# Kernel optimization log

Hardware: AMD Instinct MI355X
Metric: run time of the kernel (lower is better)

Reference implementation:

```python
import jax, jax.numpy as jnp
import numpy as np

N_FUNC, N_API = 200000, 50000
E = 400000
H = 64
L = 2


def _mean_agg(x_src, edge_index, num_dst):
    # gather source features along edges, scatter-mean onto destination nodes
    src, dst = edge_index[0], edge_index[1]
    s = jax.ops.segment_sum(x_src[src], dst, num_segments=num_dst)
    cnt = jax.ops.segment_sum(jnp.ones((dst.shape[0], 1), x_src.dtype), dst, num_segments=num_dst)
    return s / jnp.maximum(cnt, 1.0)  # zero for isolated nodes (PyG scatter-mean behavior)


def setup_inputs() -> dict:
    key = jax.random.key(0)
    ks = jax.random.split(key, 32)
    s = 0.1  # weight init scale
    inp = {
        "x_func": jax.random.normal(ks[0], (N_FUNC, 128), jnp.float32),
        "x_api": jax.random.normal(ks[1], (N_API, 64), jnp.float32),
        # input projections per node type
        "w_in_func": jax.random.normal(ks[2], (H, 128), jnp.float32) * s,
        "b_in_func": jnp.zeros((H,), jnp.float32),
        "w_in_api": jax.random.normal(ks[3], (H, 64), jnp.float32) * s,
        "b_in_api": jnp.zeros((H,), jnp.float32),
        # SAGEConv params, stacked over num_layers: lin_l (W,b) applied to aggregated msgs, lin_r (no bias) on dst
        "Wl_calls": jax.random.normal(ks[4], (L, H, H), jnp.float32) * s,
        "bl_calls": jnp.zeros((L, H), jnp.float32),
        "Wr_calls": jax.random.normal(ks[5], (L, H, H), jnp.float32) * s,
        "Wl_uses": jax.random.normal(ks[6], (L, H, H), jnp.float32) * s,
        "bl_uses": jnp.zeros((L, H), jnp.float32),
        "Wr_uses": jax.random.normal(ks[7], (L, H, H), jnp.float32) * s,
        "Wl_usedby": jax.random.normal(ks[8], (L, H, H), jnp.float32) * s,
        "bl_usedby": jnp.zeros((L, H), jnp.float32),
        "Wr_usedby": jax.random.normal(ks[9], (L, H, H), jnp.float32) * s,
        # classifier: Linear(2H -> H), ReLU, Linear(H -> 2)
        "Wc1": jax.random.normal(ks[10], (H, 2 * H), jnp.float32) * s,
        "bc1": jnp.zeros((H,), jnp.float32),
        "Wc2": jax.random.normal(ks[11], (2, H), jnp.float32) * s,
        "bc2": jnp.zeros((2,), jnp.float32),
        # edge indices: row0 = src, row1 = dst
        "ei_calls": jnp.stack([jax.random.randint(ks[12], (E,), 0, N_FUNC, jnp.int32),
                                jax.random.randint(ks[13], (E,), 0, N_FUNC, jnp.int32)]),
        "ei_uses": jnp.stack([jax.random.randint(ks[14], (E,), 0, N_FUNC, jnp.int32),
                               jax.random.randint(ks[15], (E,), 0, N_API, jnp.int32)]),
        "ei_usedby": jnp.stack([jax.random.randint(ks[16], (E,), 0, N_API, jnp.int32),
                                 jax.random.randint(ks[17], (E,), 0, N_FUNC, jnp.int32)]),
    }
    return inp


def reference(x_func, x_api, w_in_func, b_in_func, w_in_api, b_in_api,
              Wl_calls, bl_calls, Wr_calls, Wl_uses, bl_uses, Wr_uses,
              Wl_usedby, bl_usedby, Wr_usedby, Wc1, bc1, Wc2, bc2,
              ei_calls, ei_uses, ei_usedby):
    n_func, n_api = x_func.shape[0], x_api.shape[0]
    # per-node-type input projection + relu
    h_func = jax.nn.relu(x_func @ w_in_func.T + b_in_func)
    h_api = jax.nn.relu(x_api @ w_in_api.T + b_in_api)
    for l in range(L):  # small fixed layer count
        # func <- func (calls) and func <- api (used_by); HeteroConv aggr='sum'
        agg_c = _mean_agg(h_func, ei_calls, n_func)
        agg_u = _mean_agg(h_api, ei_usedby, n_func)
        out_func = (agg_c @ Wl_calls[l].T + bl_calls[l] + h_func @ Wr_calls[l].T
                    + agg_u @ Wl_usedby[l].T + bl_usedby[l] + h_func @ Wr_usedby[l].T)
        # api <- func (uses)
        agg_a = _mean_agg(h_func, ei_uses, n_api)
        out_api = agg_a @ Wl_uses[l].T + bl_uses[l] + h_api @ Wr_uses[l].T
        h_func, h_api = jax.nn.relu(out_func), jax.nn.relu(out_api)  # dropout is identity (eval)
    # per-type mean pool (single graph), concat -> classifier MLP
    pooled = jnp.concatenate([h_func.mean(0, keepdims=True), h_api.mean(0, keepdims=True)], axis=-1)
    return jax.nn.relu(pooled @ Wc1.T + bc1) @ Wc2.T + bc2  # (1, 2)
```

## Files before the change

kernel.cpp:

```cpp
#include <hip/hip_runtime.h>

#define N_FUNC 200000
#define N_API  50000
#define H      64
#define NLAYERS 2
#define NBF 3125
#define NBA 782
#define PREPB 416
#define NSHADOW 64
#define NBK   391
#define BCAP  4096
#define EPB   4096
#define WLOG_F 9
#define WLOG_A 7
#define SCAP  160

typedef unsigned short u16;
typedef unsigned int u32;
typedef __bf16 bf16x8 __attribute__((ext_vector_type(8)));
typedef float f32x4 __attribute__((ext_vector_type(4)));
typedef unsigned short u16x8 __attribute__((ext_vector_type(8)));

__device__ __forceinline__ void add4(float4& a, float4 v) {
    a.x += v.x; a.y += v.y; a.z += v.z; a.w += v.w;
}
__device__ __forceinline__ void scl4(float4& a, float s) {
    a.x *= s; a.y *= s; a.z *= s; a.w *= s;
}
__device__ __forceinline__ float bf2f(u16 u) {
    return __uint_as_float(((unsigned int)u) << 16);
}
__device__ __forceinline__ u16 f2bf(float f) {
    unsigned int x = __float_as_uint(f);
    return (u16)((x + 0x7FFFu + ((x >> 16) & 1u)) >> 16);
}
__device__ __forceinline__ ushort4 f2b4(float4 o) {
    ushort4 r; r.x = f2bf(o.x); r.y = f2bf(o.y); r.z = f2bf(o.z); r.w = f2bf(o.w);
    return r;
}
__device__ __forceinline__ void addb(float4& a, ushort4 v) {
    a.x += bf2f(v.x); a.y += bf2f(v.y); a.z += bf2f(v.z); a.w += bf2f(v.w);
}

__global__ __launch_bounds__(256, 6) void prep_and_binA(
        const float* __restrict__ w_in_func, const float* __restrict__ w_in_api,
        const float* __restrict__ Wl_calls, const float* __restrict__ Wr_calls,
        const float* __restrict__ Wl_uses,  const float* __restrict__ Wr_uses,
        const float* __restrict__ Wl_usedby,const float* __restrict__ Wr_usedby,
        u16* __restrict__ wpk,
        const int* __restrict__ sC, const int* __restrict__ dC,
        const int* __restrict__ sU, const int* __restrict__ dU,
        const int* __restrict__ sA, const int* __restrict__ dA,
        int* __restrict__ bktC, int* __restrict__ bktU, int* __restrict__ bktA,
        int* __restrict__ beC, int* __restrict__ beU, int* __restrict__ beA,
        int E, int nbPerRel)
{
    __shared__ int staged[EPB];
    __shared__ int hist[NBK + 1];
    __shared__ int lcnt[NBK];
    __shared__ int gbase[NBK];
    __shared__ int stemp[256];
    const int b = blockIdx.x, t = threadIdx.x;
    if (b < PREPB) {
        int idx = b * 256 + t;
        if (idx < 106496) {
            int half, w, K;
            const float* A; const float* B = nullptr;
            if (idx < 16384) {
                half = idx >> 13; w = idx & 8191; K = 128; A = w_in_func;
            } else if (idx < 24576) {
                int r = idx - 16384;
                half = r >> 12; w = r & 4095; K = 64; A = w_in_api;
            } else {
                int r = idx - 24576;
                int m = r >> 13;
                half = (r >> 12) & 1; w = r & 4095; K = 64;
                int l = m / 5, which = m - 5 * l;
                if (which == 0)      { A = Wr_calls  + l * 4096; B = Wr_usedby + l * 4096; }
                else if (which == 1)   A = Wl_calls  + l * 4096;
                else if (which == 2)   A = Wl_usedby + l * 4096;
                else if (which == 3)   A = Wl_uses   + l * 4096;
                else                   A = Wr_uses   + l * 4096;
            }
            int kt = w >> 11;
            int nt = (w >> 9) & 3;
            int lane = (w >> 3) & 63;
            int i = w & 7;
            int k = kt * 32 + (lane >> 4) * 8 + i;
            int n = nt * 16 + (lane & 15);
            float v = A[n * K + k];
            if (B) v += B[n * K + k];
            u16 hi = f2bf(v);
            wpk[idx] = half ? f2bf(v - bf2f(hi)) : hi;
        }
        return;
    }
    int bb = b - PREPB;
    int rel = bb / nbPerRel, lb = bb - rel * nbPerRel;
    const int* srcA; const int* dstA; int* bcnt; int* be; int wlog;
    if (rel == 0)      { srcA = sC; dstA = dC; bcnt = bktC; be = beC; wlog = WLOG_F; }
    else if (rel == 1) { srcA = sU; dstA = dU; bcnt = bktU; be = beU; wlog = WLOG_F; }
    else               { srcA = sA; dstA = dA; bcnt = bktA; be = beA; wlog = WLOG_A; }
    const int mask = (1 << wlog) - 1;
    const int e0 = lb * EPB;
    const int cnt = min(EPB, E - e0);
    for (int i = t; i < NBK; i += 256) { hist[i] = 0; lcnt[i] = 0; }
    __syncthreads();
    for (int i = t; i < cnt; i += 256)
        atomicAdd(&hist[dstA[e0 + i] >> wlog], 1);
    __syncthreads();
    int v0 = (2 * t < NBK) ? hist[2 * t] : 0;
    int v1 = (2 * t + 1 < NBK) ? hist[2 * t + 1] : 0;
    __syncthreads();
    stemp[t] = v0 + v1; __syncthreads();
    for (int s = 1; s < 256; s <<= 1) {
        int x = (t >= s) ? stemp[t - s] : 0;
        __syncthreads(); stemp[t] += x; __syncthreads();
    }
    int base = (t > 0) ? stemp[t - 1] : 0;
    if (2 * t < NBK)     hist[2 * t] = base;
    if (2 * t + 1 < NBK) hist[2 * t + 1] = base + v0;
    if (t == 255) hist[NBK] = stemp[255];
    __syncthreads();
    for (int i = t; i < cnt; i += 256) {
        int d = dstA[e0 + i], s = srcA[e0 + i];
        int bin = d >> wlog;
        int loc = atomicAdd(&lcnt[bin], 1);
        staged[hist[bin] + loc] = (s << wlog) | (d & mask);
    }
    __syncthreads();
    for (int i = t; i < NBK; i += 256) {
        int c = hist[i + 1] - hist[i];
        gbase[i] = (c > 0) ? atomicAdd(&bcnt[i], c) : 0;
    }
    __syncthreads();
    int wv = t >> 6, ln = t & 63;
    for (int bin = wv; bin < NBK; bin += 4) {
        int l0 = hist[bin], c = hist[bin + 1] - l0;
        int gb = gbase[bin];
        for (int k = ln; k < c; k += 64)
            if (gb + k < BCAP)
                be[(size_t)bin * BCAP + gb + k] = staged[l0 + k];
    }
}

__global__ __launch_bounds__(256) void scan_buckets(
        const int* __restrict__ bktC, const int* __restrict__ bktU, const int* __restrict__ bktA,
        int* __restrict__ bbC, int* __restrict__ bbU, int* __restrict__ bbA)
{
    __shared__ int st[256];
    int t = threadIdx.x;
    for (int r = 0; r < 3; ++r) {
        const int* c = (r == 0) ? bktC : (r == 1) ? bktU : bktA;
        int* B = (r == 0) ? bbC : (r == 1) ? bbU : bbA;
        int v0 = (2 * t < NBK) ? min(c[2 * t], BCAP) : 0;
        int v1 = (2 * t + 1 < NBK) ? min(c[2 * t + 1], BCAP) : 0;
        st[t] = v0 + v1; __syncthreads();
        for (int s = 1; s < 256; s <<= 1) {
            int x = (t >= s) ? st[t - s] : 0;
            __syncthreads(); st[t] += x; __syncthreads();
        }
        int base = (t > 0) ? st[t - 1] : 0;
        if (2 * t < NBK)     B[2 * t] = base;
        if (2 * t + 1 < NBK) B[2 * t + 1] = base + v0;
        __syncthreads();
    }
}

template<int K>
__device__ __forceinline__ void proj_mfma(const float* __restrict__ x,
        const u16* __restrict__ wpk, const float* __restrict__ bias,
        u16* __restrict__ hout, int i0, int nN, u16* Xb)
{
    const int t = threadIdx.x;
    const int wv = t >> 6, lane = t & 63;
    const int row = 16 * wv + (lane & 15);
    const int node = i0 + row;
    constexpr int halfOff = K * 64;
    f32x4 acc[4];
    #pragma unroll
    for (int j = 0; j < 4; ++j) acc[j] = (f32x4){0.f, 0.f, 0.f, 0.f};
    #pragma unroll
    for (int kt = 0; kt < K / 32; ++kt) {
        float v[8];
        if (node < nN) {
            const float* xp = x + (size_t)node * K + kt * 32 + (lane >> 4) * 8;
            #pragma unroll
            for (int i = 0; i < 8; ++i) v[i] = xp[i];
        } else {
            #pragma unroll
            for (int i = 0; i < 8; ++i) v[i] = 0.f;
        }
        u16x8 hh, ll;
        #pragma unroll
        for (int i = 0; i < 8; ++i) {
            u16 h = f2bf(v[i]);
            hh[i] = h;
            ll[i] = f2bf(v[i] - bf2f(h));
        }
        bf16x8 ah = __builtin_bit_cast(bf16x8, hh);
        bf16x8 al = __builtin_bit_cast(bf16x8, ll);
        #pragma unroll
        for (int nt = 0; nt < 4; ++nt) {
            bf16x8 bh = *reinterpret_cast<const bf16x8*>(wpk + (((kt * 4 + nt) * 64 + lane) << 3));
            bf16x8 bl = *reinterpret_cast<const bf16x8*>(wpk + halfOff + (((kt * 4 + nt) * 64 + lane) << 3));
            acc[nt] = __builtin_amdgcn_mfma_f32_16x16x32_bf16(ah, bh, acc[nt], 0, 0, 0);
            acc[nt] = __builtin_amdgcn_mfma_f32_16x16x32_bf16(al, bh, acc[nt], 0, 0, 0);
            acc[nt] = __builtin_amdgcn_mfma_f32_16x16x32_bf16(ah, bl, acc[nt], 0, 0, 0);
        }
    }
    #pragma unroll
    for (int nt = 0; nt < 4; ++nt) {
        int col = nt * 16 + (lane & 15);
        float bvv = bias[col];
        #pragma unroll
        for (int rg = 0; rg < 4; ++rg) {
            int r = 16 * wv + (lane >> 4) * 4 + rg;
            Xb[r * 64 + col] = f2bf(fmaxf(acc[nt][rg] + bvv, 0.f));
        }
    }
    __syncthreads();
    const int og = t & 15, ng = t >> 4;
    #pragma unroll
    for (int j = 0; j < 4; ++j) {
        int node2 = i0 + ng * 4 + j;
        if (node2 < nN) {
            ushort4 v = *reinterpret_cast<const ushort4*>(Xb + (ng * 4 + j) * 64 + og * 4);
            *reinterpret_cast<ushort4*>(hout + (size_t)node2 * H + og * 4) = v;
        }
    }
}

__global__ __launch_bounds__(256, 6) void binB_and_proj(
        const int* __restrict__ beC, const int* __restrict__ beU, const int* __restrict__ beA,
        const int* __restrict__ bktC, const int* __restrict__ bktU, const int* __restrict__ bktA,
        const int* __restrict__ bbC, const int* __restrict__ bbU, const int* __restrict__ bbA,
        int* __restrict__ rpC, int* __restrict__ rpU, int* __restrict__ rpA,
        int* __restrict__ colC, int* __restrict__ colU, int* __restrict__ colA,
        const float* __restrict__ xf, const u16* __restrict__ wpkf,
        const float* __restrict__ bf, u16* __restrict__ hf,
        const float* __restrict__ xa, const u16* __restrict__ wpka,
        const float* __restrict__ ba_, u16* __restrict__ ha)
{
    __shared__ __align__(16) int shraw[BCAP + 513 + 512];
    const int b = blockIdx.x, t = threadIdx.x;
    if (b < 3 * NBK) {
        int rel = b / NBK, bkt = b - rel * NBK;
        const int* be; const int* bc; const int* bbs; int* rp; int* col; int wlog, n;
        if (rel == 0)      { be = beC; bc = bktC; bbs = bbC; rp = rpC; col = colC; wlog = WLOG_F; n = N_FUNC; }
        else if (rel == 1) { be = beU; bc = bktU; bbs = bbU; rp = rpU; col = colU; wlog = WLOG_F; n = N_FUNC; }
        else               { be = beA; bc = bktA; bbs = bbA; rp = rpA; col = colA; wlog = WLOG_A; n = N_API; }
        const int width = 1 << wlog, mask = width - 1;
        const int nodeBase = bkt << wlog;
        const int nN = min(width, n - nodeBase);
        const int cnt = min(bc[bkt], BCAP);
        const int gb = bbs[bkt];
        int* colS = shraw;
        int* lrp  = shraw + BCAP;
        int* nxL  = shraw + BCAP + 513;
        for (int i = t; i <= 512; i += 256) { lrp[i] = 0; if (i < 512) nxL[i] = 0; }
        __syncthreads();
        const int* bePtr = be + (size_t)bkt * BCAP;
        for (int i = t; i < cnt; i += 256)
            atomicAdd(&lrp[bePtr[i] & mask], 1);
        __syncthreads();
        int v0 = lrp[2 * t], v1 = lrp[2 * t + 1];
        __syncthreads();
        int* st = colS;
        st[t] = v0 + v1; __syncthreads();
        for (int s = 1; s < 256; s <<= 1) {
            int x = (t >= s) ? st[t - s] : 0;
            __syncthreads(); st[t] += x; __syncthreads();
        }
        int base0 = (t > 0) ? st[t - 1] : 0;
        lrp[2 * t] = base0; lrp[2 * t + 1] = base0 + v0;
        if (t == 255) lrp[512] = st[255];
        __syncthreads();
        for (int i = t; i < nN; i += 256) rp[nodeBase + i] = gb + lrp[i];
        if (nodeBase + nN == n && t == 0) rp[n] = gb + lrp[nN];
        __syncthreads();
        for (int i = t; i < cnt; i += 256) {
            int en = bePtr[i]; int dl = en & mask;
            int pos = lrp[dl] + atomicAdd(&nxL[dl], 1);
            colS[pos] = en >> wlog;
        }
        __syncthreads();
        for (int i = t; i < cnt; i += 256) col[gb + i] = colS[i];
    } else {
        int b2 = b - 3 * NBK;
        u16* Xb = reinterpret_cast<u16*>(shraw);
        if (b2 < NBF) proj_mfma<128>(xf, wpkf, bf, hf, b2 * 64, N_FUNC, Xb);
        else          proj_mfma<64>(xa, wpka, ba_, ha, (b2 - NBF) * 64, N_API, Xb);
    }
}

__device__ __forceinline__ void issue_rows(const u16* __restrict__ src_h,
        const int* __restrict__ col, int c0, int c1, u16* stage, int t)
{
    const int w = t >> 6, lane = t & 63;
    const int cnt = c1 - c0;
    for (int le0 = w * 8; le0 < cnt; le0 += 32) {
        int ge = c0 + min(le0 + (lane >> 3), cnt - 1);
        int srow = col ? col[ge] : ge;
        const u16* gp = src_h + (size_t)srow * H + (lane & 7) * 8;
        __builtin_amdgcn_global_load_lds(
            (const __attribute__((address_space(1))) u32*)gp,
            (__attribute__((address_space(3))) u32*)(stage + le0 * 64),
            16, 0, 0);
    }
}

__device__ __forceinline__ void consume_rows(const u16* stage, const int s4[4],
        const int e4[4], int c0, int c1, int L, float4 acc[4])
{
    #pragma unroll
    for (int p = 0; p < 4; ++p) {
        int jlo = max(s4[p], c0), jhi = min(e4[p], c1);
        for (int j = jlo; j < jhi; ++j) {
            ushort4 v = *reinterpret_cast<const ushort4*>(stage + (size_t)(j - c0) * 64 + L * 4);
            addb(acc[p], v);
        }
    }
}

__device__ __forceinline__ void gemm_mfma_X(const u16* Xb, const u16* __restrict__ wpk,
        int wv, int lane, f32x4 acc[4])
{
    const int r = 16 * wv + (lane & 15);
    #pragma unroll
    for (int kt = 0; kt < 2; ++kt) {
        bf16x8 a = *reinterpret_cast<const bf16x8*>(
            Xb + r * 64 + (((kt * 4 + (lane >> 4)) ^ (r & 7)) << 3));
        #pragma unroll
        for (int nt = 0; nt < 4; ++nt) {
            bf16x8 bh = *reinterpret_cast<const bf16x8*>(wpk + ((kt * 256 + nt * 64 + lane) << 3));
            acc[nt] = __builtin_amdgcn_mfma_f32_16x16x32_bf16(a, bh, acc[nt], 0, 0, 0);
            bf16x8 bl = *reinterpret_cast<const bf16x8*>(wpk + 4096 + ((kt * 256 + nt * 64 + lane) << 3));
            acc[nt] = __builtin_amdgcn_mfma_f32_16x16x32_bf16(a, bl, acc[nt], 0, 0, 0);
        }
    }
}

__device__ __forceinline__ void gemm_mfma_S(const u16* stage, const u16* __restrict__ wpk,
        int wv, int lane, f32x4 acc[4])
{
    const int r = 16 * wv + (lane & 15);
    #pragma unroll
    for (int kt = 0; kt < 2; ++kt) {
        bf16x8 a = *reinterpret_cast<const bf16x8*>(
            stage + r * 64 + kt * 32 + ((lane >> 4) << 3));
        #pragma unroll
        for (int nt = 0; nt < 4; ++nt) {
            bf16x8 bh = *reinterpret_cast<const bf16x8*>(wpk + ((kt * 256 + nt * 64 + lane) << 3));
            acc[nt] = __builtin_amdgcn_mfma_f32_16x16x32_bf16(a, bh, acc[nt], 0, 0, 0);
            bf16x8 bl = *reinterpret_cast<const bf16x8*>(wpk + 4096 + ((kt * 256 + nt * 64 + lane) << 3));
            acc[nt] = __builtin_amdgcn_mfma_f32_16x16x32_bf16(a, bl, acc[nt], 0, 0, 0);
        }
    }
}

__device__ __forceinline__ void store_agg(u16* Xb, int n, int L, float4 a)
{
    *reinterpret_cast<ushort4*>(Xb + n * 64 + (((L >> 1) ^ (n & 7)) << 3) + ((L & 1) << 2)) = f2b4(a);
}

__global__ __launch_bounds__(256, 5) void layer_both(
        const u16* __restrict__ hf_old, const u16* __restrict__ ha_old,
        u16* __restrict__ hf_new, u16* __restrict__ ha_new,
        const int* __restrict__ rpC, const int* __restrict__ colC,
        const int* __restrict__ rpU, const int* __restrict__ colU,
        const int* __restrict__ rpA, const int* __restrict__ colA,
        const u16* __restrict__ pk_r, const u16* __restrict__ pk_lc,
        const u16* __restrict__ pk_lu,
        const u16* __restrict__ pk_ruse, const u16* __restrict__ pk_luse,
        const float* __restrict__ bias_c, const float* __restrict__ bias_u,
        const float* __restrict__ bias_a,
        float* __restrict__ psh)
{
    __shared__ __align__(16) u16 Xb[64 * 64];
    __shared__ __align__(16) u16 stage[SCAP * 64];
    const int b = blockIdx.x;
    const int t = threadIdx.x;
    const int L = t & 15, g = t >> 4;
    const int wv = t >> 6, lane = t & 63;
    const float4 z4 = make_float4(0.f, 0.f, 0.f, 0.f);

    f32x4 acc[4];
    #pragma unroll
    for (int j = 0; j < 4; ++j) acc[j] = (f32x4){0.f, 0.f, 0.f, 0.f};

    if (b < NBF) {
        const int i0 = b * 64;
        int s1[4], e1[4];
        #pragma unroll
        for (int p = 0; p < 4; ++p) {
            int node = i0 + p * 16 + g;
            s1[p] = rpC[node]; e1[p] = rpC[node + 1];
        }
        const int be0 = rpC[i0], be1 = rpC[i0 + 64];
        float4 a1[4];
        #pragma unroll
        for (int p = 0; p < 4; ++p) a1[p] = z4;
        for (int c0 = be0; c0 < be1; c0 += SCAP) {
            int c1 = min(c0 + SCAP, be1);
            issue_rows(hf_old, colC, c0, c1, stage, t);
            __syncthreads();
            consume_rows(stage, s1, e1, c0, c1, L, a1);
            __syncthreads();
        }
        #pragma unroll
        for (int p = 0; p < 4; ++p) {
            int n = p * 16 + g;
            scl4(a1[p], 1.0f / (float)max(e1[p] - s1[p], 1));
            store_agg(Xb, n, L, a1[p]);
        }
        __syncthreads();
        int s2[4], e2[4];
        #pragma unroll
        for (int p = 0; p < 4; ++p) {
            int node = i0 + p * 16 + g;
            s2[p] = rpU[node]; e2[p] = rpU[node + 1];
        }
        const int ue0 = rpU[i0], ue1 = rpU[i0 + 64];
        int uc1 = min(ue0 + SCAP, ue1);
        if (ue1 > ue0) issue_rows(ha_old, colU, ue0, uc1, stage, t);
        gemm_mfma_X(Xb, pk_lc, wv, lane, acc);
        __syncthreads();
        float4 a2[4];
        #pragma unroll
        for (int p = 0; p < 4; ++p) a2[p] = z4;
        if (ue1 > ue0) consume_rows(stage, s2, e2, ue0, uc1, L, a2);
        for (int c0 = uc1; c0 < ue1; c0 += SCAP) {
            int c1 = min(c0 + SCAP, ue1);
            __syncthreads();
            issue_rows(ha_old, colU, c0, c1, stage, t);
            __syncthreads();
            consume_rows(stage, s2, e2, c0, c1, L, a2);
        }
        __syncthreads();
        #pragma unroll
        for (int p = 0; p < 4; ++p) {
            int n = p * 16 + g;
            scl4(a2[p], 1.0f / (float)max(e2[p] - s2[p], 1));
            store_agg(Xb, n, L, a2[p]);
        }
        __syncthreads();
        issue_rows(hf_old, nullptr, i0, i0 + 64, stage, t);
        gemm_mfma_X(Xb, pk_lu, wv, lane, acc);
        __syncthreads();
        gemm_mfma_S(stage, pk_r, wv, lane, acc);
        #pragma unroll
        for (int nt = 0; nt < 4; ++nt) {
            int col = nt * 16 + (lane & 15);
            float bvv = bias_c[col] + bias_u[col];
            #pragma unroll
            for (int rg = 0; rg < 4; ++rg) {
                int row = 16 * wv + (lane >> 4) * 4 + rg;
                Xb[row * 64 + col] = f2bf(fmaxf(acc[nt][rg] + bvv, 0.f));
            }
        }
        __syncthreads();
        const int og = t & 15, ng = t >> 4;
        float4 s = z4;
        #pragma unroll
        for (int j = 0; j < 4; ++j) {
            int node = i0 + ng * 4 + j;
            ushort4 v = *reinterpret_cast<const ushort4*>(Xb + (ng * 4 + j) * 64 + og * 4);
            *reinterpret_cast<ushort4*>(hf_new + (size_t)node * H + og * 4) = v;
            if (psh) addb(s, v);
        }
        if (psh) {
            __syncthreads();
            float4* X4 = reinterpret_cast<float4*>(Xb);
            X4[ng * 16 + og] = s;
            __syncthreads();
            if (ng == 0) {
                float4 tot = z4;
                #pragma unroll
                for (int q = 0; q < 16; ++q) add4(tot, X4[q * 16 + og]);
                float* dst = psh + (size_t)(b & (NSHADOW - 1)) * 128 + og * 4;
                atomicAdd(dst + 0, tot.x); atomicAdd(dst + 1, tot.y);
                atomicAdd(dst + 2, tot.z); atomicAdd(dst + 3, tot.w);
            }
        }
    } else {
        const int i0 = (b - NBF) * 64;
        const int nTop = min(i0 + 64, N_API);
        int s1[4], e1[4];
        #pragma unroll
        for (int p = 0; p < 4; ++p) {
            int node = i0 + p * 16 + g;
            if (node < N_API) { s1[p] = rpA[node]; e1[p] = rpA[node + 1]; }
            else { s1[p] = 0; e1[p] = 0; }
        }
        const int be0 = rpA[i0], be1 = rpA[nTop];
        float4 a1[4];
        #pragma unroll
        for (int p = 0; p < 4; ++p) a1[p] = z4;
        for (int c0 = be0; c0 < be1; c0 += SCAP) {
            int c1 = min(c0 + SCAP, be1);
            issue_rows(hf_old, colA, c0, c1, stage, t);
            __syncthreads();
            consume_rows(stage, s1, e1, c0, c1, L, a1);
            __syncthreads();
        }
        #pragma unroll
        for (int p = 0; p < 4; ++p) {
            int n = p * 16 + g;
            scl4(a1[p], 1.0f / (float)max(e1[p] - s1[p], 1));
            store_agg(Xb, n, L, a1[p]);
        }
        __syncthreads();
        issue_rows(ha_old, nullptr, i0, nTop, stage, t);
        gemm_mfma_X(Xb, pk_luse, wv, lane, acc);
        __syncthreads();
        gemm_mfma_S(stage, pk_ruse, wv, lane, acc);
        #pragma unroll
        for (int nt = 0; nt < 4; ++nt) {
            int col = nt * 16 + (lane & 15);
            float bvv = bias_a[col];
            #pragma unroll
            for (int rg = 0; rg < 4; ++rg) {
                int row = 16 * wv + (lane >> 4) * 4 + rg;
                Xb[row * 64 + col] = f2bf(fmaxf(acc[nt][rg] + bvv, 0.f));
            }
        }
        __syncthreads();
        const int og = t & 15, ng = t >> 4;
        float4 s = z4;
        #pragma unroll
        for (int j = 0; j < 4; ++j) {
            int node = i0 + ng * 4 + j;
            if (node < N_API) {
                ushort4 v = *reinterpret_cast<const ushort4*>(Xb + (ng * 4 + j) * 64 + og * 4);
                *reinterpret_cast<ushort4*>(ha_new + (size_t)node * H + og * 4) = v;
                if (psh) addb(s, v);
            }
        }
        if (psh) {
            __syncthreads();
            float4* X4 = reinterpret_cast<float4*>(Xb);
            X4[ng * 16 + og] = s;
            __syncthreads();
            if (ng == 0) {
                float4 tot = z4;
                #pragma unroll
                for (int q = 0; q < 16; ++q) add4(tot, X4[q * 16 + og]);
                float* dst = psh + (size_t)(b & (NSHADOW - 1)) * 128 + 64 + og * 4;
                atomicAdd(dst + 0, tot.x); atomicAdd(dst + 1, tot.y);
                atomicAdd(dst + 2, tot.z); atomicAdd(dst + 3, tot.w);
            }
        }
    }
}

__global__ __launch_bounds__(128) void classifier_kernel(const float* __restrict__ shadows,
        const float* __restrict__ Wc1, const float* __restrict__ bc1,
        const float* __restrict__ Wc2, const float* __restrict__ bc2,
        float* __restrict__ out)
{
    __shared__ float ps[128];
    __shared__ float z1[64];
    int t = threadIdx.x;
    float s = 0.f;
    for (int q = 0; q < NSHADOW; ++q) s += shadows[q * 128 + t];
    ps[t] = s * (t < 64 ? (1.0f / N_FUNC) : (1.0f / N_API));
    __syncthreads();
    if (t < 64) {
        float a = bc1[t];
        for (int k = 0; k < 128; ++k) a = fmaf(ps[k], Wc1[t * 128 + k], a);
        z1[t] = fmaxf(a, 0.f);
    }
    __syncthreads();
    if (t < 2) {
        float a = bc2[t];
        for (int j = 0; j < 64; ++j) a = fmaf(z1[j], Wc2[t * 64 + j], a);
        out[t] = a;
    }
}

extern "C" void kernel_launch(void* const* d_in, const int* in_sizes, int n_in,
                              void* d_out, int out_size, void* d_ws, size_t ws_size,
                              hipStream_t stream)
{
    const float* x_func    = (const float*)d_in[0];
    const float* x_api     = (const float*)d_in[1];
    const float* w_in_func = (const float*)d_in[2];
    const float* b_in_func = (const float*)d_in[3];
    const float* w_in_api  = (const float*)d_in[4];
    const float* b_in_api  = (const float*)d_in[5];
    const float* Wl_calls  = (const float*)d_in[6];
    const float* bl_calls  = (const float*)d_in[7];
    const float* Wr_calls  = (const float*)d_in[8];
    const float* Wl_uses   = (const float*)d_in[9];
    const float* bl_uses   = (const float*)d_in[10];
    const float* Wr_uses   = (const float*)d_in[11];
    const float* Wl_usedby = (const float*)d_in[12];
    const float* bl_usedby = (const float*)d_in[13];
    const float* Wr_usedby = (const float*)d_in[14];
    const float* Wc1       = (const float*)d_in[15];
    const float* bc1       = (const float*)d_in[16];
    const float* Wc2       = (const float*)d_in[17];
    const float* bc2       = (const float*)d_in[18];
    const int*   ei_calls  = (const int*)d_in[19];
    const int*   ei_uses   = (const int*)d_in[20];
    const int*   ei_usedby = (const int*)d_in[21];
    const int E = in_sizes[19] / 2;

    float* ws = (float*)d_ws;
    size_t off = 0;
    u16* hf0 = (u16*)(ws + off); off += (size_t)N_FUNC * 32;
    u16* hf1 = (u16*)(ws + off); off += (size_t)N_FUNC * 32;
    u16* ha0 = (u16*)(ws + off); off += (size_t)N_API * 32;
    u16* ha1 = (u16*)(ws + off); off += (size_t)N_API * 32;
    u16* wpk = (u16*)(ws + off); off += 53248;
    int* bktC = (int*)(ws + off); off += NBK;
    int* bktU = (int*)(ws + off); off += NBK;
    int* bktA = (int*)(ws + off); off += NBK;
    float* shadows = ws + off; off += NSHADOW * 128;
    int* bbC = (int*)(ws + off); off += NBK;
    int* bbU = (int*)(ws + off); off += NBK;
    int* bbA = (int*)(ws + off); off += NBK;
    int* rpC = (int*)(ws + off); off += N_FUNC + 1;
    int* rpU = (int*)(ws + off); off += N_FUNC + 1;
    int* rpA = (int*)(ws + off); off += N_API + 1;
    int* colC = (int*)(ws + off); off += E;
    int* colU = (int*)(ws + off); off += E;
    int* colA = (int*)(ws + off); off += E;
    int* beC = (int*)(ws + off); off += (size_t)NBK * BCAP;
    int* beU = (int*)(ws + off); off += (size_t)NBK * BCAP;
    int* beA = (int*)(ws + off); off += (size_t)NBK * BCAP;

    const int nbPerRel = (E + EPB - 1) / EPB;

    hipMemsetAsync(bktC, 0, (size_t)(3 * NBK + NSHADOW * 128) * sizeof(float), stream);

    prep_and_binA<<<PREPB + 3 * nbPerRel, 256, 0, stream>>>(
            w_in_func, w_in_api, Wl_calls, Wr_calls, Wl_uses, Wr_uses,
            Wl_usedby, Wr_usedby, wpk,
            ei_calls, ei_calls + E, ei_usedby, ei_usedby + E, ei_uses, ei_uses + E,
            bktC, bktU, bktA, beC, beU, beA, E, nbPerRel);

    scan_buckets<<<1, 256, 0, stream>>>(bktC, bktU, bktA, bbC, bbU, bbA);

    u16* wpkf = wpk;
    u16* wpka = wpk + 16384;
    u16* wpkL = wpk + 24576;
    u16 *pk_r[NLAYERS], *pk_lc[NLAYERS], *pk_lu[NLAYERS], *pk_luse[NLAYERS], *pk_ruse[NLAYERS];
    for (int l = 0; l < NLAYERS; ++l) {
        pk_r[l]    = wpkL + (size_t)(l * 5 + 0) * 8192;
        pk_lc[l]   = wpkL + (size_t)(l * 5 + 1) * 8192;
        pk_lu[l]   = wpkL + (size_t)(l * 5 + 2) * 8192;
        pk_luse[l] = wpkL + (size_t)(l * 5 + 3) * 8192;
        pk_ruse[l] = wpkL + (size_t)(l * 5 + 4) * 8192;
    }

    binB_and_proj<<<3 * NBK + NBF + NBA, 256, 0, stream>>>(
            beC, beU, beA, bktC, bktU, bktA, bbC, bbU, bbA,
            rpC, rpU, rpA, colC, colU, colA,
            x_func, wpkf, b_in_func, hf0,
            x_api, wpka, b_in_api, ha0);

    u16* hf[2] = { hf0, hf1 };
    u16* ha[2] = { ha0, ha1 };
    for (int l = 0; l < NLAYERS; ++l) {
        int cur = l & 1, nxt = cur ^ 1;
        layer_both<<<NBF + NBA, 256, 0, stream>>>(
                hf[cur], ha[cur], hf[nxt], ha[nxt],
                rpC, colC, rpU, colU, rpA, colA,
                pk_r[l], pk_lc[l], pk_lu[l], pk_ruse[l], pk_luse[l],
                bl_calls + l * 64, bl_usedby + l * 64, bl_uses + l * 64,
                (l == NLAYERS - 1) ? shadows : nullptr);
    }

    classifier_kernel<<<1, 128, 0, stream>>>(shadows, Wc1, bc1, Wc2, bc2, (float*)d_out);
}
```

Before: 205.4 us.

## Double-buffer edge-row gathers and load self rows directly into registers

Result: slower. 219.4 us (+6.8%).

```diff
diff --git a/kernel.cpp b/kernel.cpp
--- a/kernel.cpp
+++ b/kernel.cpp
@@ -13,7 +13,8 @@
 #define EPB   4096
 #define WLOG_F 9
 #define WLOG_A 7
-#define SCAP  160
+#define SCAP_H 80
+#define HOFF (SCAP_H * 64)
 
 typedef unsigned short u16;
 typedef unsigned int u32;
@@ -295,29 +296,29 @@
 }
 
 __device__ __forceinline__ void issue_rows(const u16* __restrict__ src_h,
-        const int* __restrict__ col, int c0, int c1, u16* stage, int t)
+        const int* __restrict__ col, int c0, int c1, u16* half_base, int t)
 {
     const int w = t >> 6, lane = t & 63;
     const int cnt = c1 - c0;
     for (int le0 = w * 8; le0 < cnt; le0 += 32) {
         int ge = c0 + min(le0 + (lane >> 3), cnt - 1);
-        int srow = col ? col[ge] : ge;
+        int srow = col[ge];
         const u16* gp = src_h + (size_t)srow * H + (lane & 7) * 8;
         __builtin_amdgcn_global_load_lds(
             (const __attribute__((address_space(1))) u32*)gp,
-            (__attribute__((address_space(3))) u32*)(stage + le0 * 64),
+            (__attribute__((address_space(3))) u32*)(half_base + le0 * 64),
             16, 0, 0);
     }
 }
 
-__device__ __forceinline__ void consume_rows(const u16* stage, const int s4[4],
+__device__ __forceinline__ void consume_rows(const u16* half_base, const int s4[4],
         const int e4[4], int c0, int c1, int L, float4 acc[4])
 {
     #pragma unroll
     for (int p = 0; p < 4; ++p) {
         int jlo = max(s4[p], c0), jhi = min(e4[p], c1);
         for (int j = jlo; j < jhi; ++j) {
-            ushort4 v = *reinterpret_cast<const ushort4*>(stage + (size_t)(j - c0) * 64 + L * 4);
+            ushort4 v = *reinterpret_cast<const ushort4*>(half_base + (size_t)(j - c0) * 64 + L * 4);
             addb(acc[p], v);
         }
     }
@@ -341,20 +342,17 @@
     }
 }
 
-__device__ __forceinline__ void gemm_mfma_S(const u16* stage, const u16* __restrict__ wpk,
-        int wv, int lane, f32x4 acc[4])
-{
-    const int r = 16 * wv + (lane & 15);
+__device__ __forceinline__ void gemm_mfma_R(const bf16x8 ao[2], const u16* __restrict__ wpk,
+        int lane, f32x4 acc[4])
+{
     #pragma unroll
     for (int kt = 0; kt < 2; ++kt) {
-        bf16x8 a = *reinterpret_cast<const bf16x8*>(
-            stage + r * 64 + kt * 32 + ((lane >> 4) << 3));
         #pragma unroll
         for (int nt = 0; nt < 4; ++nt) {
             bf16x8 bh = *reinterpret_cast<const bf16x8*>(wpk + ((kt * 256 + nt * 64 + lane) << 3));
-            acc[nt] = __builtin_amdgcn_mfma_f32_16x16x32_bf16(a, bh, acc[nt], 0, 0, 0);
+            acc[nt] = __builtin_amdgcn_mfma_f32_16x16x32_bf16(ao[kt], bh, acc[nt], 0, 0, 0);
             bf16x8 bl = *reinterpret_cast<const bf16x8*>(wpk + 4096 + ((kt * 256 + nt * 64 + lane) << 3));
-            acc[nt] = __builtin_amdgcn_mfma_f32_16x16x32_bf16(a, bl, acc[nt], 0, 0, 0);
+            acc[nt] = __builtin_amdgcn_mfma_f32_16x16x32_bf16(ao[kt], bl, acc[nt], 0, 0, 0);
         }
     }
 }
@@ -378,7 +376,7 @@
         float* __restrict__ psh)
 {
     __shared__ __align__(16) u16 Xb[64 * 64];
-    __shared__ __align__(16) u16 stage[SCAP * 64];
+    __shared__ __align__(16) u16 stage[2 * SCAP_H * 64];
     const int b = blockIdx.x;
     const int t = threadIdx.x;
     const int L = t & 15, g = t >> 4;
@@ -388,31 +386,44 @@
     f32x4 acc[4];
     #pragma unroll
     for (int j = 0; j < 4; ++j) acc[j] = (f32x4){0.f, 0.f, 0.f, 0.f};
+    int buf = 0;
 
     if (b < NBF) {
         const int i0 = b * 64;
+        bf16x8 ao[2];
+        {
+            int r = 16 * wv + (lane & 15);
+            #pragma unroll
+            for (int kt = 0; kt < 2; ++kt)
+                ao[kt] = *reinterpret_cast<const bf16x8*>(
+                    hf_old + (size_t)(i0 + r) * H + kt * 32 + ((lane >> 4) << 3));
+        }
         int s1[4], e1[4];
         #pragma unroll
         for (int p = 0; p < 4; ++p) {
             int node = i0 + p * 16 + g;
             s1[p] = rpC[node]; e1[p] = rpC[node + 1];
         }
-        const int be0 = rpC[i0], be1 = rpC[i0 + 64];
-        float4 a1[4];
-        #pragma unroll
-        for (int p = 0; p < 4; ++p) a1[p] = z4;
-        for (int c0 = be0; c0 < be1; c0 += SCAP) {
-            int c1 = min(c0 + SCAP, be1);
-            issue_rows(hf_old, colC, c0, c1, stage, t);
-            __syncthreads();
-            consume_rows(stage, s1, e1, c0, c1, L, a1);
-            __syncthreads();
-        }
-        #pragma unroll
-        for (int p = 0; p < 4; ++p) {
-            int n = p * 16 + g;
-            scl4(a1[p], 1.0f / (float)max(e1[p] - s1[p], 1));
-            store_agg(Xb, n, L, a1[p]);
+        {
+            const int be0 = rpC[i0], be1 = rpC[i0 + 64];
+            float4 a1[4];
+            #pragma unroll
+            for (int p = 0; p < 4; ++p) a1[p] = z4;
+            int c0 = be0, c1 = min(c0 + SCAP_H, be1);
+            if (c0 < be1) issue_rows(hf_old, colC, c0, c1, stage + buf * HOFF, t);
+            while (c0 < be1) {
+                __syncthreads();
+                int n0 = c1, n1 = min(n0 + SCAP_H, be1);
+                if (n0 < be1) issue_rows(hf_old, colC, n0, n1, stage + (buf ^ 1) * HOFF, t);
+                consume_rows(stage + buf * HOFF, s1, e1, c0, c1, L, a1);
+                c0 = n0; c1 = n1; buf ^= 1;
+            }
+            #pragma unroll
+            for (int p = 0; p < 4; ++p) {
+                int n = p * 16 + g;
+                scl4(a1[p], 1.0f / (float)max(e1[p] - s1[p], 1));
+                store_agg(Xb, n, L, a1[p]);
+            }
         }
         __syncthreads();
         int s2[4], e2[4];
@@ -422,33 +433,32 @@
             s2[p] = rpU[node]; e2[p] = rpU[node + 1];
         }
         const int ue0 = rpU[i0], ue1 = rpU[i0 + 64];
-        int uc1 = min(ue0 + SCAP, ue1);
-        if (ue1 > ue0) issue_rows(ha_old, colU, ue0, uc1, stage, t);
+        int c0 = ue0, c1 = min(c0 + SCAP_H, ue1);
+        if (c0 < ue1) issue_rows(ha_old, colU, c0, c1, stage + buf * HOFF, t);
         gemm_mfma_X(Xb, pk_lc, wv, lane, acc);
-        __syncthreads();
-        float4 a2[4];
-        #pragma unroll
-        for (int p = 0; p < 4; ++p) a2[p] = z4;
-        if (ue1 > ue0) consume_rows(stage, s2, e2, ue0, uc1, L, a2);
-        for (int c0 = uc1; c0 < ue1; c0 += SCAP) {
-            int c1 = min(c0 + SCAP, ue1);
+        {
+            float4 a2[4];
+            #pragma unroll
+            for (int p = 0; p < 4; ++p) a2[p] = z4;
+            while (c0 < ue1) {
+                __syncthreads();
+                int n0 = c1, n1 = min(n0 + SCAP_H, ue1);
+                if (n0 < ue1) issue_rows(ha_old, colU, n0, n1, stage + (buf ^ 1) * HOFF, t);
+                consume_rows(stage + buf * HOFF, s2, e2, c0, c1, L, a2);
+                c0 = n0; c1 = n1; buf ^= 1;
+            }
             __syncthreads();
-            issue_rows(ha_old, colU, c0, c1, stage, t);
-            __syncthreads();
-            consume_rows(stage, s2, e2, c0, c1, L, a2);
-        }
-        __syncthreads();
-        #pragma unroll
-        for (int p = 0; p < 4; ++p) {
-            int n = p * 16 + g;
-            scl4(a2[p], 1.0f / (float)max(e2[p] - s2[p], 1));
-            store_agg(Xb, n, L, a2[p]);
-        }
-        __syncthreads();
-        issue_rows(hf_old, nullptr, i0, i0 + 64, stage, t);
+            #pragma unroll
+            for (int p = 0; p < 4; ++p) {
+                int n = p * 16 + g;
+                scl4(a2[p], 1.0f / (float)max(e2[p] - s2[p], 1));
+                store_agg(Xb, n, L, a2[p]);
+            }
+        }
+        __syncthreads();
         gemm_mfma_X(Xb, pk_lu, wv, lane, acc);
-        __syncthreads();
-        gemm_mfma_S(stage, pk_r, wv, lane, acc);
+        gemm_mfma_R(ao, pk_r, lane, acc);
+        __syncthreads();
         #pragma unroll
         for (int nt = 0; nt < 4; ++nt) {
             int col = nt * 16 + (lane & 15);
@@ -486,6 +496,20 @@
     } else {
         const int i0 = (b - NBF) * 64;
         const int nTop = min(i0 + 64, N_API);
+        bf16x8 ao[2];
+        {
+            int r = 16 * wv + (lane & 15);
+            #pragma unroll
+            for (int kt = 0; kt < 2; ++kt) {
+                if (i0 + r < N_API) {
+                    ao[kt] = *reinterpret_cast<const bf16x8*>(
+                        ha_old + (size_t)(i0 + r) * H + kt * 32 + ((lane >> 4) << 3));
+                } else {
+                    u16x8 zz = (u16x8){0, 0, 0, 0, 0, 0, 0, 0};
+                    ao[kt] = __builtin_bit_cast(bf16x8, zz);
+                }
+            }
+        }
         int s1[4], e1[4];
         #pragma unroll
         for (int p = 0; p < 4; ++p) {
@@ -493,28 +517,31 @@
             if (node < N_API) { s1[p] = rpA[node]; e1[p] = rpA[node + 1]; }
             else { s1[p] = 0; e1[p] = 0; }
         }
-        const int be0 = rpA[i0], be1 = rpA[nTop];
-        float4 a1[4];
-        #pragma unroll
-        for (int p = 0; p < 4; ++p) a1[p] = z4;
-        for (int c0 = be0; c0 < be1; c0 += SCAP) {
-            int c1 = min(c0 + SCAP, be1);
-            issue_rows(hf_old, colA, c0, c1, stage, t);
-            __syncthreads();
-            consume_rows(stage, s1, e1, c0, c1, L, a1);
-            __syncthreads();
-        }
-        #pragma unroll
-        for (int p = 0; p < 4; ++p) {
-            int n = p * 16 + g;
-            scl4(a1[p], 1.0f / (float)max(e1[p] - s1[p], 1));
-            store_agg(Xb, n, L, a1[p]);
-        }
-        __syncthreads();
-        issue_rows(ha_old, nullptr, i0, nTop, stage, t);
+        {
+            const int be0 = rpA[i0], be1 = rpA[nTop];
+            float4 a1[4];
+            #pragma unroll
+            for (int p = 0; p < 4; ++p) a1[p] = z4;
+            int c0 = be0, c1 = min(c0 + SCAP_H, be1);
+            if (c0 < be1) issue_rows(hf_old, colA, c0, c1, stage + buf * HOFF, t);
+            while (c0 < be1) {
+                __syncthreads();
+                int n0 = c1, n1 = min(n0 + SCAP_H, be1);
+                if (n0 < be1) issue_rows(hf_old, colA, n0, n1, stage + (buf ^ 1) * HOFF, t);
+                consume_rows(stage + buf * HOFF, s1, e1, c0, c1, L, a1);
+                c0 = n0; c1 = n1; buf ^= 1;
+            }
+            #pragma unroll
+            for (int p = 0; p < 4; ++p) {
+                int n = p * 16 + g;
+                scl4(a1[p], 1.0f / (float)max(e1[p] - s1[p], 1));
+                store_agg(Xb, n, L, a1[p]);
+            }
+        }
+        __syncthreads();
         gemm_mfma_X(Xb, pk_luse, wv, lane, acc);
-        __syncthreads();
-        gemm_mfma_S(stage, pk_ruse, wv, lane, acc);
+        gemm_mfma_R(ao, pk_ruse, lane, acc);
+        __syncthreads();
         #pragma unroll
         for (int nt = 0; nt < 4; ++nt) {
             int col = nt * 16 + (lane & 15);
```

## Give each wave its own gather staging slice to drop block-wide barriers

Applied to the files above, without the earlier changes.

After: 229.8 us. 1.12x slower.

```diff
diff --git a/kernel.cpp b/kernel.cpp
--- a/kernel.cpp
+++ b/kernel.cpp
@@ -13,7 +13,8 @@
 #define EPB   4096
 #define WLOG_F 9
 #define WLOG_A 7
-#define SCAP  160
+#define SCAP_W 24
+#define WSLOT (SCAP_W + 16)
 
 typedef unsigned short u16;
 typedef unsigned int u32;
@@ -294,32 +295,30 @@
     }
 }
 
-__device__ __forceinline__ void issue_rows(const u16* __restrict__ src_h,
-        const int* __restrict__ col, int c0, int c1, u16* stage, int t)
-{
-    const int w = t >> 6, lane = t & 63;
+__device__ __forceinline__ void issue_rows_wave(const u16* __restrict__ src_h,
+        const int* __restrict__ col, int c0, int c1, u16* wslice, int lane)
+{
     const int cnt = c1 - c0;
-    for (int le0 = w * 8; le0 < cnt; le0 += 32) {
+    for (int le0 = 0; le0 < cnt; le0 += 8) {
         int ge = c0 + min(le0 + (lane >> 3), cnt - 1);
         int srow = col ? col[ge] : ge;
         const u16* gp = src_h + (size_t)srow * H + (lane & 7) * 8;
         __builtin_amdgcn_global_load_lds(
             (const __attribute__((address_space(1))) u32*)gp,
-            (__attribute__((address_space(3))) u32*)(stage + le0 * 64),
+            (__attribute__((address_space(3))) u32*)(wslice + le0 * 64),
             16, 0, 0);
     }
 }
 
-__device__ __forceinline__ void consume_rows(const u16* stage, const int s4[4],
-        const int e4[4], int c0, int c1, int L, float4 acc[4])
-{
-    #pragma unroll
-    for (int p = 0; p < 4; ++p) {
-        int jlo = max(s4[p], c0), jhi = min(e4[p], c1);
-        for (int j = jlo; j < jhi; ++j) {
-            ushort4 v = *reinterpret_cast<const ushort4*>(stage + (size_t)(j - c0) * 64 + L * 4);
-            addb(acc[p], v);
-        }
+__device__ __forceinline__ void consume_wave(const u16* wslice, int s_e, int e_e,
+        int c0, int c1, int dqq, float4 a[4])
+{
+    int jlo = max(s_e, c0), jhi = min(e_e, c1);
+    for (int j = jlo; j < jhi; ++j) {
+        const u16* rowp = wslice + (size_t)(j - c0) * 64 + dqq * 16;
+        #pragma unroll
+        for (int q = 0; q < 4; ++q)
+            addb(a[q], *reinterpret_cast<const ushort4*>(rowp + q * 4));
     }
 }
 
@@ -341,14 +340,14 @@
     }
 }
 
-__device__ __forceinline__ void gemm_mfma_S(const u16* stage, const u16* __restrict__ wpk,
-        int wv, int lane, f32x4 acc[4])
-{
-    const int r = 16 * wv + (lane & 15);
+__device__ __forceinline__ void gemm_mfma_W(const u16* wown, const u16* __restrict__ wpk,
+        int lane, f32x4 acc[4])
+{
+    const int rr = lane & 15;
     #pragma unroll
     for (int kt = 0; kt < 2; ++kt) {
         bf16x8 a = *reinterpret_cast<const bf16x8*>(
-            stage + r * 64 + kt * 32 + ((lane >> 4) << 3));
+            wown + rr * 64 + kt * 32 + ((lane >> 4) << 3));
         #pragma unroll
         for (int nt = 0; nt < 4; ++nt) {
             bf16x8 bh = *reinterpret_cast<const bf16x8*>(wpk + ((kt * 256 + nt * 64 + lane) << 3));
@@ -378,77 +377,79 @@
         float* __restrict__ psh)
 {
     __shared__ __align__(16) u16 Xb[64 * 64];
-    __shared__ __align__(16) u16 stage[SCAP * 64];
+    __shared__ __align__(16) u16 stage[4 * WSLOT * 64];
     const int b = blockIdx.x;
     const int t = threadIdx.x;
-    const int L = t & 15, g = t >> 4;
     const int wv = t >> 6, lane = t & 63;
     const float4 z4 = make_float4(0.f, 0.f, 0.f, 0.f);
+
+    u16* wg  = stage + wv * (WSLOT * 64);
+    u16* wow = wg + SCAP_W * 64;
 
     f32x4 acc[4];
     #pragma unroll
     for (int j = 0; j < 4; ++j) acc[j] = (f32x4){0.f, 0.f, 0.f, 0.f};
 
+    const int dqq = lane & 3;
+
     if (b < NBF) {
         const int i0 = b * 64;
-        int s1[4], e1[4];
-        #pragma unroll
-        for (int p = 0; p < 4; ++p) {
-            int node = i0 + p * 16 + g;
-            s1[p] = rpC[node]; e1[p] = rpC[node + 1];
-        }
-        const int be0 = rpC[i0], be1 = rpC[i0 + 64];
-        float4 a1[4];
-        #pragma unroll
-        for (int p = 0; p < 4; ++p) a1[p] = z4;
-        for (int c0 = be0; c0 < be1; c0 += SCAP) {
-            int c1 = min(c0 + SCAP, be1);
-            issue_rows(hf_old, colC, c0, c1, stage, t);
-            __syncthreads();
-            consume_rows(stage, s1, e1, c0, c1, L, a1);
-            __syncthreads();
-        }
-        #pragma unroll
-        for (int p = 0; p < 4; ++p) {
-            int n = p * 16 + g;
-            scl4(a1[p], 1.0f / (float)max(e1[p] - s1[p], 1));
-            store_agg(Xb, n, L, a1[p]);
-        }
-        __syncthreads();
-        int s2[4], e2[4];
-        #pragma unroll
-        for (int p = 0; p < 4; ++p) {
-            int node = i0 + p * 16 + g;
-            s2[p] = rpU[node]; e2[p] = rpU[node + 1];
-        }
-        const int ue0 = rpU[i0], ue1 = rpU[i0 + 64];
-        int uc1 = min(ue0 + SCAP, ue1);
-        if (ue1 > ue0) issue_rows(ha_old, colU, ue0, uc1, stage, t);
+        const int nw0 = i0 + 16 * wv;
+        const int node = nw0 + (lane >> 2);
+        issue_rows_wave(hf_old, nullptr, nw0, nw0 + 16, wow, lane);
+        int s1 = rpC[node], e1 = rpC[node + 1];
+        const int ws1 = rpC[nw0], we1 = rpC[nw0 + 16];
+        float4 a1[4] = {z4, z4, z4, z4};
+        int c0 = ws1, c1 = min(c0 + SCAP_W, we1);
+        if (c0 < we1) issue_rows_wave(hf_old, colC, c0, c1, wg, lane);
+        while (c0 < we1) {
+            asm volatile("s_waitcnt vmcnt(0)" ::: "memory");
+            consume_wave(wg, s1, e1, c0, c1, dqq, a1);
+            asm volatile("s_waitcnt lgkmcnt(0)" ::: "memory");
+            c0 = c1;
+            if (c0 < we1) {
+                c1 = min(c0 + SCAP_W, we1);
+                issue_rows_wave(hf_old, colC, c0, c1, wg, lane);
+            }
+        }
+        {
+            float rs = 1.0f / (float)max(e1 - s1, 1);
+            #pragma unroll
+            for (int q = 0; q < 4; ++q) {
+                scl4(a1[q], rs);
+                store_agg(Xb, node - i0, dqq * 4 + q, a1[q]);
+            }
+        }
+        __syncthreads();
+        int s2 = rpU[node], e2 = rpU[node + 1];
+        const int ws2 = rpU[nw0], we2 = rpU[nw0 + 16];
+        c0 = ws2; c1 = min(c0 + SCAP_W, we2);
+        if (c0 < we2) issue_rows_wave(ha_old, colU, c0, c1, wg, lane);
         gemm_mfma_X(Xb, pk_lc, wv, lane, acc);
-        __syncthreads();
-        float4 a2[4];
-        #pragma unroll
-        for (int p = 0; p < 4; ++p) a2[p] = z4;
-        if (ue1 > ue0) consume_rows(stage, s2, e2, ue0, uc1, L, a2);
-        for (int c0 = uc1; c0 < ue1; c0 += SCAP) {
-            int c1 = min(c0 + SCAP, ue1);
-            __syncthreads();
-            issue_rows(ha_old, colU, c0, c1, stage, t);
-            __syncthreads();
-            consume_rows(stage, s2, e2, c0, c1, L, a2);
-        }
-        __syncthreads();
-        #pragma unroll
-        for (int p = 0; p < 4; ++p) {
-            int n = p * 16 + g;
-            scl4(a2[p], 1.0f / (float)max(e2[p] - s2[p], 1));
-            store_agg(Xb, n, L, a2[p]);
-        }
-        __syncthreads();
-        issue_rows(hf_old, nullptr, i0, i0 + 64, stage, t);
+        float4 a2[4] = {z4, z4, z4, z4};
+        while (c0 < we2) {
+            asm volatile("s_waitcnt vmcnt(0)" ::: "memory");
+            consume_wave(wg, s2, e2, c0, c1, dqq, a2);
+            asm volatile("s_waitcnt lgkmcnt(0)" ::: "memory");
+            c0 = c1;
+            if (c0 < we2) {
+                c1 = min(c0 + SCAP_W, we2);
+                issue_rows_wave(ha_old, colU, c0, c1, wg, lane);
+            }
+        }
+        __syncthreads();
+        {
+            float rs = 1.0f / (float)max(e2 - s2, 1);
+            #pragma unroll
+            for (int q = 0; q < 4; ++q) {
+                scl4(a2[q], rs);
+                store_agg(Xb, node - i0, dqq * 4 + q, a2[q]);
+            }
+        }
+        __syncthreads();
         gemm_mfma_X(Xb, pk_lu, wv, lane, acc);
-        __syncthreads();
-        gemm_mfma_S(stage, pk_r, wv, lane, acc);
+        gemm_mfma_W(wow, pk_r, lane, acc);
+        __syncthreads();
         #pragma unroll
         for (int nt = 0; nt < 4; ++nt) {
             int col = nt * 16 + (lane & 15);
@@ -464,9 +465,9 @@
         float4 s = z4;
         #pragma unroll
         for (int j = 0; j < 4; ++j) {
-            int node = i0 + ng * 4 + j;
+            int node2 = i0 + ng * 4 + j;
             ushort4 v = *reinterpret_cast<const ushort4*>(Xb + (ng * 4 + j) * 64 + og * 4);
-            *reinterpret_cast<ushort4*>(hf_new + (size_t)node * H + og * 4) = v;
+            *reinterpret_cast<ushort4*>(hf_new + (size_t)node2 * H + og * 4) = v;
             if (psh) addb(s, v);
         }
         if (psh) {
@@ -485,36 +486,40 @@
         }
     } else {
         const int i0 = (b - NBF) * 64;
-        const int nTop = min(i0 + 64, N_API);
-        int s1[4], e1[4];
-        #pragma unroll
-        for (int p = 0; p < 4; ++p) {
-            int node = i0 + p * 16 + g;
-            if (node < N_API) { s1[p] = rpA[node]; e1[p] = rpA[node + 1]; }
-            else { s1[p] = 0; e1[p] = 0; }
-        }
-        const int be0 = rpA[i0], be1 = rpA[nTop];
-        float4 a1[4];
-        #pragma unroll
-        for (int p = 0; p < 4; ++p) a1[p] = z4;
-        for (int c0 = be0; c0 < be1; c0 += SCAP) {
-            int c1 = min(c0 + SCAP, be1);
-            issue_rows(hf_old, colA, c0, c1, stage, t);
-            __syncthreads();
-            consume_rows(stage, s1, e1, c0, c1, L, a1);
-            __syncthreads();
-        }
-        #pragma unroll
-        for (int p = 0; p < 4; ++p) {
-            int n = p * 16 + g;
-            scl4(a1[p], 1.0f / (float)max(e1[p] - s1[p], 1));
-            store_agg(Xb, n, L, a1[p]);
-        }
-        __syncthreads();
-        issue_rows(ha_old, nullptr, i0, nTop, stage, t);
+        const int nw0 = i0 + 16 * wv;
+        const int node = nw0 + (lane >> 2);
+        {
+            int c0o = min(nw0, N_API), c1o = min(nw0 + 16, N_API);
+            if (c0o < c1o) issue_rows_wave(ha_old, nullptr, c0o, c1o, wow, lane);
+        }
+        int s1 = 0, e1 = 0;
+        if (node < N_API) { s1 = rpA[node]; e1 = rpA[node + 1]; }
+        const int ws1 = rpA[min(nw0, N_API)], we1 = rpA[min(nw0 + 16, N_API)];
+        float4 a1[4] = {z4, z4, z4, z4};
+        int c0 = ws1, c1 = min(c0 + SCAP_W, we1);
+        if (c0 < we1) issue_rows_wave(hf_old, colA, c0, c1, wg, lane);
+        while (c0 < we1) {
+            asm volatile("s_waitcnt vmcnt(0)" ::: "memory");
+            consume_wave(wg, s1, e1, c0, c1, dqq, a1);
+            asm volatile("s_waitcnt lgkmcnt(0)" ::: "memory");
+            c0 = c1;
+            if (c0 < we1) {
+                c1 = min(c0 + SCAP_W, we1);
+                issue_rows_wave(hf_old, colA, c0, c1, wg, lane);
+            }
+        }
+        {
+            float rs = 1.0f / (float)max(e1 - s1, 1);
+            #pragma unroll
+            for (int q = 0; q < 4; ++q) {
+                scl4(a1[q], rs);
+                store_agg(Xb, node - i0, dqq * 4 + q, a1[q]);
+            }
+        }
+        __syncthreads();
         gemm_mfma_X(Xb, pk_luse, wv, lane, acc);
-        __syncthreads();
-        gemm_mfma_S(stage, pk_ruse, wv, lane, acc);
+        gemm_mfma_W(wow, pk_ruse, lane, acc);
+        __syncthreads();
         #pragma unroll
         for (int nt = 0; nt < 4; ++nt) {
             int col = nt * 16 + (lane & 15);
@@ -530,10 +535,10 @@
         float4 s = z4;
         #pragma unroll
         for (int j = 0; j < 4; ++j) {
-            int node = i0 + ng * 4 + j;
-            if (node < N_API) {
+            int node2 = i0 + ng * 4 + j;
+            if (node2 < N_API) {
                 ushort4 v = *reinterpret_cast<const ushort4*>(Xb + (ng * 4 + j) * 64 + og * 4);
-                *reinterpret_cast<ushort4*>(ha_new + (size_t)node * H + og * 4) = v;
+                *reinterpret_cast<ushort4*>(ha_new + (size_t)node2 * H + og * 4) = v;
                 if (psh) addb(s, v);
             }
         }
```
